# Performance work log

Hardware: AMD Instinct MI355X
Metric: run time of the kernel (lower is better)

## Reference

```python
import jax, jax.numpy as jnp
import numpy as np
import math

EMBED_DIM = 2048
NUM_HEADS = 16
D_K = 128
BSZ = 2
SEQ = 2048


def make_freq_pos_enc(dim, max_seq_len):
    # inv_freq over dim/2 freqs, then interleave-repeat each freq twice: (f r), r=2
    inv_freq = 1.0 / (10000.0 ** (jnp.arange(0, dim, 2, dtype=jnp.float32) / dim))
    pos = jnp.arange(max_seq_len, dtype=jnp.float32)
    pe = jnp.einsum('p,f->pf', pos, inv_freq)                 # [S, dim/2]
    return jnp.repeat(pe, 2, axis=-1)                          # [S, dim], pattern (f r)


def rotate_half(u):
    # pairs are interleaved: (..., d r) with r=2
    u = u.reshape(*u.shape[:-1], -1, 2)
    u1, u2 = u[..., 0], u[..., 1]
    return jnp.stack((-u2, u1), axis=-1).reshape(*u.shape[:-2], -1)


def rotate(u, pos_enc):
    pe = pos_enc[: u.shape[-2]]                                # [S, d_k]
    return u * jnp.cos(pe) + rotate_half(u) * jnp.sin(pe)


def setup_inputs() -> dict:
    key = jax.random.key(0)
    ks = jax.random.split(key, 5)
    scale = 1.0 / math.sqrt(EMBED_DIM)
    return {
        'x': jax.random.normal(ks[0], (BSZ, SEQ, EMBED_DIM), dtype=jnp.float32),
        'wq': jax.random.normal(ks[1], (NUM_HEADS * D_K, EMBED_DIM), dtype=jnp.float32) * scale,
        'wk': jax.random.normal(ks[2], (NUM_HEADS * D_K, EMBED_DIM), dtype=jnp.float32) * scale,
        'wv': jax.random.normal(ks[3], (NUM_HEADS * D_K, EMBED_DIM), dtype=jnp.float32) * scale,
        'wo': jax.random.normal(ks[4], (EMBED_DIM, NUM_HEADS * D_K), dtype=jnp.float32) * scale,
        'freq_pos_enc': make_freq_pos_enc(D_K, SEQ),
        'mask': jnp.zeros((SEQ, SEQ), dtype=jnp.float32),  # dead arg in original forward
        'num_heads': NUM_HEADS,
        'd_k': D_K,
    }


def reference(x, wq, wk, wv, wo, freq_pos_enc, mask, num_heads, d_k):
    bsz, seq_len, _ = x.shape
    # projections (nn.Linear, no bias): x @ W^T
    def proj(w):
        p = jnp.einsum('bse,de->bsd', x, w)
        return p.reshape(bsz, seq_len, num_heads, d_k).transpose(0, 2, 1, 3)  # [B,H,S,d]
    q, k, v = proj(wq), proj(wk), proj(wv)
    q, k = rotate(q, freq_pos_enc), rotate(k, freq_pos_enc)
    # regenerated causal mask (0 on/below diagonal, -inf above)
    causal = jnp.where(
        jnp.arange(seq_len)[:, None] >= jnp.arange(seq_len)[None, :],
        0.0, -jnp.inf).astype(x.dtype)
    scores = jnp.einsum('bhsd,bhtd->bhst', q, k) / math.sqrt(d_k) + causal
    weights = jax.nn.softmax(scores, axis=-1)
    attn = jnp.einsum('bhst,bhtd->bhsd', weights, v)           # [B,H,S,d]
    attn = attn.transpose(0, 2, 1, 3).reshape(bsz, seq_len, -1)
    return jnp.einsum('bsd,ed->bse', attn, wo)


if __name__ == '__main__':
    out = reference(**setup_inputs())
    print(out.shape, out.dtype)
```

## Files before the change

### kernel.cpp

```cpp
#include <hip/hip_runtime.h>


typedef unsigned short u16;
typedef unsigned int   u32;
typedef __attribute__((ext_vector_type(4)))  float f32x4;
typedef __attribute__((ext_vector_type(16))) float f32x16;
typedef __attribute__((ext_vector_type(8)))  short short8;
typedef __attribute__((ext_vector_type(4)))  u16   u16x4;
typedef __attribute__((ext_vector_type(2)))  u16   u16x2;

#define NB   2
#define NH   16
#define SEQ  2048
#define DK   128
#define EMB  2048

__device__ __forceinline__ u16 f2bf(float f) {
    union { float f; unsigned int u; } v; v.f = f;
    unsigned int r = v.u + 0x7FFFu + ((v.u >> 16) & 1u);
    return (u16)(r >> 16);
}
__device__ __forceinline__ float bf2f(u16 h) {
    union { unsigned int u; float f; } v; v.u = ((unsigned int)h) << 16;
    return v.f;
}
__device__ __forceinline__ f32x4 mfma16(short8 a, short8 b, f32x4 c) {
    return __builtin_amdgcn_mfma_f32_16x16x32_bf16(a, b, c, 0, 0, 0);
}
__device__ __forceinline__ f32x16 mfma32(short8 a, short8 b, f32x16 c) {
    return __builtin_amdgcn_mfma_f32_32x32x16_bf16(a, b, c, 0, 0, 0);
}

#define GLDS(gsrc, ldst) __builtin_amdgcn_global_load_lds( \
    (const __attribute__((address_space(1))) void*)(gsrc), \
    (__attribute__((address_space(3))) void*)(ldst), 16, 0, 0)

__global__ __launch_bounds__(256) void cast_f32_bf16(const float* __restrict__ in,
                                                     u16* __restrict__ out, int n4) {
    int i = blockIdx.x * 256 + threadIdx.x;
    if (i >= n4) return;
    f32x4 v = ((const f32x4*)in)[i];
    u16x4 o;
    o[0] = f2bf(v[0]); o[1] = f2bf(v[1]); o[2] = f2bf(v[2]); o[3] = f2bf(v[3]);
    ((u16x4*)out)[i] = o;
}

__global__ __launch_bounds__(256) void rope_table(const float* __restrict__ freq,
                                                  float* __restrict__ ct,
                                                  float* __restrict__ st) {
    int i = blockIdx.x * 256 + threadIdx.x;
    int s = i >> 6, d2 = i & 63;
    float pe = freq[s * DK + d2 * 2];
    ct[i] = cosf(pe);
    st[i] = sinf(pe);
}

__global__ __launch_bounds__(256) void rope_apply(u16* __restrict__ Qb, u16* __restrict__ Kb,
                                                  const float* __restrict__ ct,
                                                  const float* __restrict__ st) {
    int i = blockIdx.x * 256 + threadIdx.x;
    int d2 = i & 63;
    int s  = (i >> 6) & (SEQ - 1);
    float c  = ct[(s << 6) + d2];
    float sn = st[(s << 6) + d2];
    size_t off = (size_t)i * 2;
    u16x2 q = *(const u16x2*)(Qb + off);
    float q0 = bf2f(q[0]), q1 = bf2f(q[1]);
    u16x2 qo; qo[0] = f2bf(q0 * c - q1 * sn); qo[1] = f2bf(q1 * c + q0 * sn);
    *(u16x2*)(Qb + off) = qo;
    u16x2 k = *(const u16x2*)(Kb + off);
    float k0 = bf2f(k[0]), k1 = bf2f(k[1]);
    u16x2 ko; ko[0] = f2bf(k0 * c - k1 * sn); ko[1] = f2bf(k1 * c + k0 * sn);
    *(u16x2*)(Kb + off) = ko;
}

template <int MODE>
__global__ __launch_bounds__(256) void gemm_ring(const u16* __restrict__ A,
                                                 const u16* __restrict__ B,
                                                 void* __restrict__ Cout,
                                                 int M, int N, int K) {
    __shared__ __align__(16) u16 As[3 * 4096];
    __shared__ __align__(16) u16 Bs[3 * 4096];
    const int tid  = threadIdx.x;
    const int lane = tid & 63;
    const int wid  = tid >> 6;
    const int wm   = wid >> 1, wn = wid & 1;
    const int nwgx = (int)gridDim.x;
    const int wgid = (int)blockIdx.y * nwgx + (int)blockIdx.x;
    const int cpx  = (nwgx * (int)gridDim.y) >> 3;
    const int swz  = (wgid & 7) * cpx + (wgid >> 3);
    const int m0   = (swz % nwgx) * 128, n0 = (swz / nwgx) * 128;
    const int lr   = lane & 15, lk = lane >> 4;

    const u16* Asrc = A + (size_t)(m0 + (tid >> 2)) * K + (tid & 3) * 8;
    const u16* Bsrc = B + (size_t)(n0 + (tid >> 2)) * K + (tid & 3) * 8;
    const int  dst0 = wid * 512;

    f32x4 acc[4][4] = {};
    const int NT = K >> 5;

#pragma unroll
    for (int i = 0; i < 2; ++i) {
        GLDS(Asrc + (size_t)i * 64 * K,      &As[i * 2048 + dst0]);
        GLDS(Bsrc + (size_t)i * 64 * K,      &Bs[i * 2048 + dst0]);
    }
#pragma unroll
    for (int i = 0; i < 2; ++i) {
        GLDS(Asrc + (size_t)i * 64 * K + 32, &As[4096 + i * 2048 + dst0]);
        GLDS(Bsrc + (size_t)i * 64 * K + 32, &Bs[4096 + i * 2048 + dst0]);
    }

    int buf = 0;
    for (int t = 0; t < NT; ++t) {
        if (t < NT - 1) asm volatile("s_waitcnt vmcnt(4)" ::: "memory");
        else            asm volatile("s_waitcnt vmcnt(0)" ::: "memory");
        __builtin_amdgcn_s_barrier();

        short8 af[4], bf[4];
#pragma unroll
        for (int i = 0; i < 4; ++i)
            af[i] = *(const short8*)&As[buf * 4096 + (wm * 64 + i * 16 + lr) * 32 + lk * 8];
#pragma unroll
        for (int j = 0; j < 4; ++j)
            bf[j] = *(const short8*)&Bs[buf * 4096 + (wn * 64 + j * 16 + lr) * 32 + lk * 8];

        if (t + 2 < NT) {
            int b2 = buf + 2; if (b2 >= 3) b2 -= 3;
            const u16* a2  = Asrc + (size_t)(t + 2) * 32;
            const u16* b2p = Bsrc + (size_t)(t + 2) * 32;
#pragma unroll
            for (int i = 0; i < 2; ++i) {
                GLDS(a2  + (size_t)i * 64 * K, &As[b2 * 4096 + i * 2048 + dst0]);
                GLDS(b2p + (size_t)i * 64 * K, &Bs[b2 * 4096 + i * 2048 + dst0]);
            }
        }

        __builtin_amdgcn_s_setprio(1);
#pragma unroll
        for (int i = 0; i < 4; ++i)
#pragma unroll
            for (int j = 0; j < 4; ++j)
                acc[i][j] = mfma16(af[i], bf[j], acc[i][j]);
        __builtin_amdgcn_s_setprio(0);

        buf = (buf == 2) ? 0 : buf + 1;
    }

#pragma unroll
    for (int i = 0; i < 4; ++i) {
#pragma unroll
        for (int j = 0; j < 4; ++j) {
#pragma unroll
            for (int r = 0; r < 4; ++r) {
                int m = m0 + wm * 64 + i * 16 + lk * 4 + r;
                int n = n0 + wn * 64 + j * 16 + lr;
                float v = acc[i][j][r];
                if (MODE == 0) {
                    int b = m >> 11, s = m & (SEQ - 1), h = n >> 7, d = n & (DK - 1);
                    ((u16*)Cout)[(((size_t)(b * NH + h) * SEQ + s) * DK) + d] = f2bf(v);
                } else if (MODE == 1) {
                    int h = m >> 7, d = m & (DK - 1), b = n >> 11, s = n & (SEQ - 1);
                    ((u16*)Cout)[(((size_t)(b * NH + h) * DK + d) * SEQ) + s] = f2bf(v);
                } else {
                    ((float*)Cout)[(size_t)m * N + n] = v;
                }
            }
        }
    }
}

__global__ __launch_bounds__(128, 2) void attn_lds2(const u16* __restrict__ Q,
                                                    const u16* __restrict__ K,
                                                    const u16* __restrict__ VT,
                                                    u16* __restrict__ O) {
    const int gid  = blockIdx.x;
    const int bh   = (gid & 7) * 4 + ((gid >> 3) & 3);
    const int p    = gid >> 5;
    const int tid  = threadIdx.x;
    const int w    = tid >> 6;
    const int l    = tid & 63;
    const int q32  = l & 31;
    const int half = l >> 5;
    const int qcL  = 63 - p;
    const int qc   = w ? p : qcL;
    const int nt   = qcL + 1;
    const int q0   = qc * 32;

    __shared__ __align__(16) u16 Ksh[2][4096];
    __shared__ __align__(16) u16 Vsh[2][4096];

    const u16* Kg  = K  + (size_t)bh * SEQ * DK;
    const u16* VTg = VT + (size_t)bh * DK * SEQ;
    const int b = bh >> 4, h = bh & 15;

    auto stage = [&](int t, int bufn) {
#pragma unroll
        for (int i = 0; i < 4; ++i) {
            int cid = i * 128 + w * 64 + l;
            int kr = cid >> 4, kc = cid & 15;
            GLDS(Kg + (size_t)(t * 32 + kr) * DK + ((kc ^ (kr & 7)) * 8),
                 &Ksh[bufn][(i * 128 + w * 64) * 8]);
            int vr = cid >> 2, vc = cid & 3;
            GLDS(VTg + (size_t)vr * SEQ + t * 32 + ((vc ^ ((vr >> 1) & 3)) * 8),
                 &Vsh[bufn][(i * 128 + w * 64) * 8]);
        }
    };

    short8 qf[8];
    {
        const u16* Qg = Q + ((size_t)bh * SEQ + q0) * DK;
#pragma unroll
        for (int kq = 0; kq < 8; ++kq)
            qf[kq] = *(const short8*)(Qg + q32 * DK + kq * 16 + half * 8);
    }

    f32x16 oacc[4] = {};
    float m = -INFINITY, lsum = 0.f;

    stage(0, 0);
    stage(1, 1);
    for (int t = 0; t < nt; ++t) {
        const int buf = t & 1;
        if (t + 1 < nt) asm volatile("s_waitcnt vmcnt(8)" ::: "memory");
        else            asm volatile("s_waitcnt vmcnt(0)" ::: "memory");
        __builtin_amdgcn_s_barrier();
        __builtin_amdgcn_sched_barrier(0);

        if (t <= qc) {
            const float rs = 0.08838834764831845f;
            short8 kf[8], vf[8];
#pragma unroll
            for (int kq = 0; kq < 8; ++kq) {
                int c = (kq * 2 + half) ^ (q32 & 7);
                kf[kq] = *(const short8*)&Ksh[buf][q32 * 128 + c * 8];
            }
#pragma unroll
            for (int i = 0; i < 8; ++i) {
                int dblk = i >> 1, ch = i & 1;
                int vrow = dblk * 32 + q32;
                int c = (ch * 2 + half) ^ ((q32 >> 1) & 3);
                vf[i] = *(const short8*)&Vsh[buf][vrow * 32 + c * 8];
            }
            const bool diag = (t == qc);

            f32x16 sacc = {};
            __builtin_amdgcn_s_setprio(1);
#pragma unroll
            for (int kq = 0; kq < 8; ++kq) sacc = mfma32(kf[kq], qf[kq], sacc);
            __builtin_amdgcn_s_setprio(0);
#pragma unroll
            for (int r = 0; r < 16; ++r) {
                int kk = (r & 3) + 8 * (r >> 2) + 4 * half;
                float s = sacc[r] * rs;
                if (diag && kk > q32) s = -INFINITY;
                sacc[r] = s;
            }
            float mx[8];
#pragma unroll
            for (int r = 0; r < 8; ++r) mx[r] = fmaxf(sacc[r], sacc[r + 8]);
#pragma unroll
            for (int r = 0; r < 4; ++r) mx[r] = fmaxf(mx[r], mx[r + 4]);
            float tmax = fmaxf(fmaxf(mx[0], mx[1]), fmaxf(mx[2], mx[3]));
            tmax = fmaxf(tmax, __shfl_xor(tmax, 32));
            if (__any(tmax - m > 8.0f)) {
                float mn = fmaxf(m, tmax);
                float sc = __expf(m - mn);
                m = mn; lsum *= sc;
#pragma unroll
                for (int d = 0; d < 4; ++d)
#pragma unroll
                    for (int r = 0; r < 16; ++r) oacc[d][r] *= sc;
            }
#pragma unroll
            for (int r = 0; r < 16; ++r) sacc[r] = __expf(sacc[r] - m);
            float sm[8];
#pragma unroll
            for (int r = 0; r < 8; ++r) sm[r] = sacc[r] + sacc[r + 8];
#pragma unroll
            for (int r = 0; r < 4; ++r) sm[r] = sm[r] + sm[r + 4];
            float tsum = (sm[0] + sm[1]) + (sm[2] + sm[3]);
            tsum += __shfl_xor(tsum, 32);
            lsum += tsum;
            u32 pk[8];
#pragma unroll
            for (int i = 0; i < 8; ++i)
                pk[i] = ((u32)f2bf(sacc[2 * i + 1]) << 16) | (u32)f2bf(sacc[2 * i]);
            u32 s0 = __shfl_xor((int)pk[0], 32), s1 = __shfl_xor((int)pk[1], 32);
            u32 s2 = __shfl_xor((int)pk[2], 32), s3 = __shfl_xor((int)pk[3], 32);
            u32 s4 = __shfl_xor((int)pk[4], 32), s5 = __shfl_xor((int)pk[5], 32);
            u32 s6 = __shfl_xor((int)pk[6], 32), s7 = __shfl_xor((int)pk[7], 32);
            union { u32 wd[4]; short8 s8; } P0, P1;
            P0.wd[0] = half ? s2    : pk[0];  P0.wd[1] = half ? s3    : pk[1];
            P0.wd[2] = half ? pk[2] : s0;     P0.wd[3] = half ? pk[3] : s1;
            P1.wd[0] = half ? s6    : pk[4];  P1.wd[1] = half ? s7    : pk[5];
            P1.wd[2] = half ? pk[6] : s4;     P1.wd[3] = half ? pk[7] : s5;
            __builtin_amdgcn_s_setprio(1);
#pragma unroll
            for (int d = 0; d < 4; ++d) {
                oacc[d] = mfma32(vf[2 * d],     P0.s8, oacc[d]);
                oacc[d] = mfma32(vf[2 * d + 1], P1.s8, oacc[d]);
            }
            __builtin_amdgcn_s_setprio(0);
        }

        __builtin_amdgcn_s_barrier();
        if (t + 2 < nt) stage(t + 2, buf);
    }

    float inv = 1.0f / lsum;
    u16* Og = O + ((size_t)b * SEQ + q0 + q32) * EMB + h * DK;
#pragma unroll
    for (int d = 0; d < 4; ++d)
#pragma unroll
        for (int rq = 0; rq < 4; ++rq) {
            u16x4 o4;
#pragma unroll
            for (int j = 0; j < 4; ++j) o4[j] = f2bf(oacc[d][rq * 4 + j] * inv);
            *(u16x4*)(Og + d * 32 + rq * 8 + half * 4) = o4;
        }
}

extern "C" void kernel_launch(void* const* d_in, const int* in_sizes, int n_in,
                              void* d_out, int out_size, void* d_ws, size_t ws_size,
                              hipStream_t stream) {
    const float* x    = (const float*)d_in[0];
    const float* wq   = (const float*)d_in[1];
    const float* wk   = (const float*)d_in[2];
    const float* wv   = (const float*)d_in[3];
    const float* wo   = (const float*)d_in[4];
    const float* freq = (const float*)d_in[5];

    char* ws = (char*)d_ws;
    u16*  xb  = (u16*)(ws);
    u16*  wqb = (u16*)(ws + 16777216);
    u16*  wkb = (u16*)(ws + 25165824);
    u16*  wvb = (u16*)(ws + 33554432);
    u16*  wob = (u16*)(ws + 41943040);
    u16*  Qb  = (u16*)(ws + 50331648);
    u16*  Kb  = (u16*)(ws + 67108864);
    u16*  VTb = (u16*)(ws + 83886080);
    float* ct = (float*)(ws + 100663296);
    float* st = (float*)(ws + 101187584);
    u16*  attn = xb;

    cast_f32_bf16<<<8192, 256, 0, stream>>>(x,  xb,  2097152);
    cast_f32_bf16<<<4096, 256, 0, stream>>>(wq, wqb, 1048576);
    cast_f32_bf16<<<4096, 256, 0, stream>>>(wk, wkb, 1048576);
    cast_f32_bf16<<<4096, 256, 0, stream>>>(wv, wvb, 1048576);
    cast_f32_bf16<<<4096, 256, 0, stream>>>(wo, wob, 1048576);
    rope_table<<<512, 256, 0, stream>>>(freq, ct, st);

    gemm_ring<0><<<dim3(32, 16), 256, 0, stream>>>(xb,  wqb, Qb,  4096, 2048, 2048);
    gemm_ring<0><<<dim3(32, 16), 256, 0, stream>>>(xb,  wkb, Kb,  4096, 2048, 2048);
    gemm_ring<1><<<dim3(16, 32), 256, 0, stream>>>(wvb, xb,  VTb, 2048, 4096, 2048);

    rope_apply<<<16384, 256, 0, stream>>>(Qb, Kb, ct, st);

    attn_lds2<<<1024, 128, 0, stream>>>(Qb, Kb, VTb, attn);

    gemm_ring<3><<<dim3(32, 16), 256, 0, stream>>>(attn, wob, d_out, 4096, 2048, 2048);
}
```

Before: 294.5 us.

## Use 64-key tiles with adjacent query-chunk pairs in attention; merge weight casts

The attention kernel now pairs two adjacent 32-row query chunks per block and stages 64-key K/V tiles, replacing the earlier pairing of a long and a short chunk. This halves the number of loop iterations and barriers per block and lets both waves share each staged tile, at the cost of doubled LDS per buffer and more registers. Blocks are launched in reverse order so the longest ones start first. Separately, the four weight-cast launches are merged into a single kernel to cut launch overhead.

```diff
diff --git a/kernel.cpp b/kernel.cpp
--- a/kernel.cpp
+++ b/kernel.cpp
@@ -43,6 +43,23 @@
     u16x4 o;
     o[0] = f2bf(v[0]); o[1] = f2bf(v[1]); o[2] = f2bf(v[2]); o[3] = f2bf(v[3]);
     ((u16x4*)out)[i] = o;
+}
+
+__global__ __launch_bounds__(256) void cast_weights(const float* __restrict__ wq,
+                                                    const float* __restrict__ wk,
+                                                    const float* __restrict__ wv,
+                                                    const float* __restrict__ wo,
+                                                    u16* __restrict__ oq, u16* __restrict__ ok,
+                                                    u16* __restrict__ ov, u16* __restrict__ oo) {
+    int i   = blockIdx.x * 256 + threadIdx.x;
+    int sel = i >> 20;
+    int idx = i & 1048575;
+    const float* src = (sel == 0) ? wq : (sel == 1) ? wk : (sel == 2) ? wv : wo;
+    u16*         dst = (sel == 0) ? oq : (sel == 1) ? ok : (sel == 2) ? ov : oo;
+    f32x4 v = ((const f32x4*)src)[idx];
+    u16x4 o;
+    o[0] = f2bf(v[0]); o[1] = f2bf(v[1]); o[2] = f2bf(v[2]); o[3] = f2bf(v[3]);
+    ((u16x4*)dst)[idx] = o;
 }
 
 __global__ __launch_bounds__(256) void rope_table(const float* __restrict__ freq,
@@ -169,46 +186,45 @@
     }
 }
 
-__global__ __launch_bounds__(128, 2) void attn_lds2(const u16* __restrict__ Q,
-                                                    const u16* __restrict__ K,
-                                                    const u16* __restrict__ VT,
-                                                    u16* __restrict__ O) {
+__global__ __launch_bounds__(128, 2) void attn64(const u16* __restrict__ Q,
+                                                 const u16* __restrict__ K,
+                                                 const u16* __restrict__ VT,
+                                                 u16* __restrict__ O) {
     const int gid  = blockIdx.x;
     const int bh   = (gid & 7) * 4 + ((gid >> 3) & 3);
-    const int p    = gid >> 5;
+    const int p    = 31 - (gid >> 5);
     const int tid  = threadIdx.x;
     const int w    = tid >> 6;
     const int l    = tid & 63;
     const int q32  = l & 31;
     const int half = l >> 5;
-    const int qcL  = 63 - p;
-    const int qc   = w ? p : qcL;
-    const int nt   = qcL + 1;
-    const int q0   = qc * 32;
-
-    __shared__ __align__(16) u16 Ksh[2][4096];
-    __shared__ __align__(16) u16 Vsh[2][4096];
+    const int qc   = 2 * p + w;
+    const int q    = qc * 32 + q32;
+    const int nt   = p + 1;
+
+    __shared__ __align__(16) u16 Ksh[2][8192];
+    __shared__ __align__(16) u16 Vsh[2][8192];
 
     const u16* Kg  = K  + (size_t)bh * SEQ * DK;
     const u16* VTg = VT + (size_t)bh * DK * SEQ;
     const int b = bh >> 4, h = bh & 15;
 
-    auto stage = [&](int t, int bufn) {
-#pragma unroll
-        for (int i = 0; i < 4; ++i) {
+    auto stage = [&](int T, int bufn) {
+#pragma unroll
+        for (int i = 0; i < 8; ++i) {
             int cid = i * 128 + w * 64 + l;
             int kr = cid >> 4, kc = cid & 15;
-            GLDS(Kg + (size_t)(t * 32 + kr) * DK + ((kc ^ (kr & 7)) * 8),
+            GLDS(Kg + (size_t)(T * 64 + kr) * DK + ((kc ^ (kr & 7)) * 8),
                  &Ksh[bufn][(i * 128 + w * 64) * 8]);
-            int vr = cid >> 2, vc = cid & 3;
-            GLDS(VTg + (size_t)vr * SEQ + t * 32 + ((vc ^ ((vr >> 1) & 3)) * 8),
+            int vr = cid >> 3, vc = cid & 7;
+            GLDS(VTg + (size_t)vr * SEQ + T * 64 + ((vc ^ (vr & 7)) * 8),
                  &Vsh[bufn][(i * 128 + w * 64) * 8]);
         }
     };
 
     short8 qf[8];
     {
-        const u16* Qg = Q + ((size_t)bh * SEQ + q0) * DK;
+        const u16* Qg = Q + ((size_t)bh * SEQ + qc * 32) * DK;
 #pragma unroll
         for (int kq = 0; kq < 8; ++kq)
             qf[kq] = *(const short8*)(Qg + q32 * DK + kq * 16 + half * 8);
@@ -221,94 +237,140 @@
     stage(1, 1);
     for (int t = 0; t < nt; ++t) {
         const int buf = t & 1;
-        if (t + 1 < nt) asm volatile("s_waitcnt vmcnt(8)" ::: "memory");
+        if (t + 1 < nt) asm volatile("s_waitcnt vmcnt(16)" ::: "memory");
         else            asm volatile("s_waitcnt vmcnt(0)" ::: "memory");
         __builtin_amdgcn_s_barrier();
         __builtin_amdgcn_sched_barrier(0);
 
-        if (t <= qc) {
-            const float rs = 0.08838834764831845f;
-            short8 kf[8], vf[8];
+        const float rs = 0.08838834764831845f;
+        const bool diag = (t == p);
+        const bool doH1 = !(diag && w == 0);
+
+        short8 kf[8];
+#pragma unroll
+        for (int kq = 0; kq < 8; ++kq) {
+            int c = (kq * 2 + half) ^ (q32 & 7);
+            kf[kq] = *(const short8*)&Ksh[buf][q32 * 128 + c * 8];
+        }
+        f32x16 sacc0 = {};
+        __builtin_amdgcn_s_setprio(1);
+#pragma unroll
+        for (int kq = 0; kq < 8; ++kq) sacc0 = mfma32(kf[kq], qf[kq], sacc0);
+        __builtin_amdgcn_s_setprio(0);
+
+        f32x16 sacc1 = {};
+        if (doH1) {
 #pragma unroll
             for (int kq = 0; kq < 8; ++kq) {
                 int c = (kq * 2 + half) ^ (q32 & 7);
-                kf[kq] = *(const short8*)&Ksh[buf][q32 * 128 + c * 8];
+                kf[kq] = *(const short8*)&Ksh[buf][(32 + q32) * 128 + c * 8];
             }
-#pragma unroll
-            for (int i = 0; i < 8; ++i) {
-                int dblk = i >> 1, ch = i & 1;
-                int vrow = dblk * 32 + q32;
-                int c = (ch * 2 + half) ^ ((q32 >> 1) & 3);
-                vf[i] = *(const short8*)&Vsh[buf][vrow * 32 + c * 8];
+            __builtin_amdgcn_s_setprio(1);
+#pragma unroll
+            for (int kq = 0; kq < 8; ++kq) sacc1 = mfma32(kf[kq], qf[kq], sacc1);
+            __builtin_amdgcn_s_setprio(0);
+        }
+
+#pragma unroll
+        for (int r = 0; r < 16; ++r) {
+            int kk = 64 * t + (r & 3) + 8 * (r >> 2) + 4 * half;
+            float s0 = sacc0[r] * rs;
+            if (diag && kk > q) s0 = -INFINITY;
+            sacc0[r] = s0;
+            float s1 = sacc1[r] * rs;
+            if (diag && kk + 32 > q) s1 = -INFINITY;
+            sacc1[r] = s1;
+        }
+
+        float mx[8];
+#pragma unroll
+        for (int r = 0; r < 8; ++r) mx[r] = fmaxf(sacc0[r], sacc0[r + 8]);
+        if (doH1) {
+#pragma unroll
+            for (int r = 0; r < 8; ++r) mx[r] = fmaxf(mx[r], fmaxf(sacc1[r], sacc1[r + 8]));
+        }
+#pragma unroll
+        for (int r = 0; r < 4; ++r) mx[r] = fmaxf(mx[r], mx[r + 4]);
+        float tmax = fmaxf(fmaxf(mx[0], mx[1]), fmaxf(mx[2], mx[3]));
+        tmax = fmaxf(tmax, __shfl_xor(tmax, 32));
+        if (__any(tmax - m > 8.0f)) {
+            float mn = fmaxf(m, tmax);
+            float sc = __expf(m - mn);
+            m = mn; lsum *= sc;
+#pragma unroll
+            for (int d = 0; d < 4; ++d)
+#pragma unroll
+                for (int r = 0; r < 16; ++r) oacc[d][r] *= sc;
+        }
+#pragma unroll
+        for (int r = 0; r < 16; ++r) sacc0[r] = __expf(sacc0[r] - m);
+        if (doH1) {
+#pragma unroll
+            for (int r = 0; r < 16; ++r) sacc1[r] = __expf(sacc1[r] - m);
+        }
+        float sm[8];
+#pragma unroll
+        for (int r = 0; r < 8; ++r) sm[r] = sacc0[r] + sacc0[r + 8];
+        if (doH1) {
+#pragma unroll
+            for (int r = 0; r < 8; ++r) sm[r] += sacc1[r] + sacc1[r + 8];
+        }
+#pragma unroll
+        for (int r = 0; r < 4; ++r) sm[r] = sm[r] + sm[r + 4];
+        float tsum = (sm[0] + sm[1]) + (sm[2] + sm[3]);
+        tsum += __shfl_xor(tsum, 32);
+        lsum += tsum;
+
+        u32 pk[8];
+#pragma unroll
+        for (int i = 0; i < 8; ++i)
+            pk[i] = ((u32)f2bf(sacc0[2 * i + 1]) << 16) | (u32)f2bf(sacc0[2 * i]);
+        u32 s0 = __shfl_xor((int)pk[0], 32), s1 = __shfl_xor((int)pk[1], 32);
+        u32 s2 = __shfl_xor((int)pk[2], 32), s3 = __shfl_xor((int)pk[3], 32);
+        u32 s4 = __shfl_xor((int)pk[4], 32), s5 = __shfl_xor((int)pk[5], 32);
+        u32 s6 = __shfl_xor((int)pk[6], 32), s7 = __shfl_xor((int)pk[7], 32);
+        union { u32 wd[4]; short8 s8; } P0, P1, P2, P3;
+        P0.wd[0] = half ? s2    : pk[0];  P0.wd[1] = half ? s3    : pk[1];
+        P0.wd[2] = half ? pk[2] : s0;     P0.wd[3] = half ? pk[3] : s1;
+        P1.wd[0] = half ? s6    : pk[4];  P1.wd[1] = half ? s7    : pk[5];
+        P1.wd[2] = half ? pk[6] : s4;     P1.wd[3] = half ? pk[7] : s5;
+        if (doH1) {
+#pragma unroll
+            for (int i = 0; i < 8; ++i)
+                pk[i] = ((u32)f2bf(sacc1[2 * i + 1]) << 16) | (u32)f2bf(sacc1[2 * i]);
+            u32 t0 = __shfl_xor((int)pk[0], 32), t1 = __shfl_xor((int)pk[1], 32);
+            u32 t2 = __shfl_xor((int)pk[2], 32), t3 = __shfl_xor((int)pk[3], 32);
+            u32 t4 = __shfl_xor((int)pk[4], 32), t5 = __shfl_xor((int)pk[5], 32);
+            u32 t6 = __shfl_xor((int)pk[6], 32), t7 = __shfl_xor((int)pk[7], 32);
+            P2.wd[0] = half ? t2    : pk[0];  P2.wd[1] = half ? t3    : pk[1];
+            P2.wd[2] = half ? pk[2] : t0;     P2.wd[3] = half ? pk[3] : t1;
+            P3.wd[0] = half ? t6    : pk[4];  P3.wd[1] = half ? t7    : pk[5];
+            P3.wd[2] = half ? pk[6] : t4;     P3.wd[3] = half ? pk[7] : t5;
+        }
+
+        __builtin_amdgcn_s_setprio(1);
+#pragma unroll
+        for (int d = 0; d < 4; ++d) {
+            int vrow = d * 32 + q32;
+            short8 v0 = *(const short8*)&Vsh[buf][vrow * 64 + (((0 * 2 + half) ^ (q32 & 7)) * 8)];
+            short8 v1 = *(const short8*)&Vsh[buf][vrow * 64 + (((1 * 2 + half) ^ (q32 & 7)) * 8)];
+            oacc[d] = mfma32(v0, P0.s8, oacc[d]);
+            oacc[d] = mfma32(v1, P1.s8, oacc[d]);
+            if (doH1) {
+                short8 v2 = *(const short8*)&Vsh[buf][vrow * 64 + (((2 * 2 + half) ^ (q32 & 7)) * 8)];
+                short8 v3 = *(const short8*)&Vsh[buf][vrow * 64 + (((3 * 2 + half) ^ (q32 & 7)) * 8)];
+                oacc[d] = mfma32(v2, P2.s8, oacc[d]);
+                oacc[d] = mfma32(v3, P3.s8, oacc[d]);
             }
-            const bool diag = (t == qc);
-
-            f32x16 sacc = {};
-            __builtin_amdgcn_s_setprio(1);
-#pragma unroll
-            for (int kq = 0; kq < 8; ++kq) sacc = mfma32(kf[kq], qf[kq], sacc);
-            __builtin_amdgcn_s_setprio(0);
-#pragma unroll
-            for (int r = 0; r < 16; ++r) {
-                int kk = (r & 3) + 8 * (r >> 2) + 4 * half;
-                float s = sacc[r] * rs;
-                if (diag && kk > q32) s = -INFINITY;
-                sacc[r] = s;
-            }
-            float mx[8];
-#pragma unroll
-            for (int r = 0; r < 8; ++r) mx[r] = fmaxf(sacc[r], sacc[r + 8]);
-#pragma unroll
-            for (int r = 0; r < 4; ++r) mx[r] = fmaxf(mx[r], mx[r + 4]);
-            float tmax = fmaxf(fmaxf(mx[0], mx[1]), fmaxf(mx[2], mx[3]));
-            tmax = fmaxf(tmax, __shfl_xor(tmax, 32));
-            if (__any(tmax - m > 8.0f)) {
-                float mn = fmaxf(m, tmax);
-                float sc = __expf(m - mn);
-                m = mn; lsum *= sc;
-#pragma unroll
-                for (int d = 0; d < 4; ++d)
-#pragma unroll
-                    for (int r = 0; r < 16; ++r) oacc[d][r] *= sc;
-            }
-#pragma unroll
-            for (int r = 0; r < 16; ++r) sacc[r] = __expf(sacc[r] - m);
-            float sm[8];
-#pragma unroll
-            for (int r = 0; r < 8; ++r) sm[r] = sacc[r] + sacc[r + 8];
-#pragma unroll
-            for (int r = 0; r < 4; ++r) sm[r] = sm[r] + sm[r + 4];
-            float tsum = (sm[0] + sm[1]) + (sm[2] + sm[3]);
-            tsum += __shfl_xor(tsum, 32);
-            lsum += tsum;
-            u32 pk[8];
-#pragma unroll
-            for (int i = 0; i < 8; ++i)
-                pk[i] = ((u32)f2bf(sacc[2 * i + 1]) << 16) | (u32)f2bf(sacc[2 * i]);
-            u32 s0 = __shfl_xor((int)pk[0], 32), s1 = __shfl_xor((int)pk[1], 32);
-            u32 s2 = __shfl_xor((int)pk[2], 32), s3 = __shfl_xor((int)pk[3], 32);
-            u32 s4 = __shfl_xor((int)pk[4], 32), s5 = __shfl_xor((int)pk[5], 32);
-            u32 s6 = __shfl_xor((int)pk[6], 32), s7 = __shfl_xor((int)pk[7], 32);
-            union { u32 wd[4]; short8 s8; } P0, P1;
-            P0.wd[0] = half ? s2    : pk[0];  P0.wd[1] = half ? s3    : pk[1];
-            P0.wd[2] = half ? pk[2] : s0;     P0.wd[3] = half ? pk[3] : s1;
-            P1.wd[0] = half ? s6    : pk[4];  P1.wd[1] = half ? s7    : pk[5];
-            P1.wd[2] = half ? pk[6] : s4;     P1.wd[3] = half ? pk[7] : s5;
-            __builtin_amdgcn_s_setprio(1);
-#pragma unroll
-            for (int d = 0; d < 4; ++d) {
-                oacc[d] = mfma32(vf[2 * d],     P0.s8, oacc[d]);
-                oacc[d] = mfma32(vf[2 * d + 1], P1.s8, oacc[d]);
-            }
-            __builtin_amdgcn_s_setprio(0);
-        }
+        }
+        __builtin_amdgcn_s_setprio(0);
 
         __builtin_amdgcn_s_barrier();
         if (t + 2 < nt) stage(t + 2, buf);
     }
 
     float inv = 1.0f / lsum;
-    u16* Og = O + ((size_t)b * SEQ + q0 + q32) * EMB + h * DK;
+    u16* Og = O + ((size_t)b * SEQ + qc * 32 + q32) * EMB + h * DK;
 #pragma unroll
     for (int d = 0; d < 4; ++d)
 #pragma unroll
@@ -343,11 +405,8 @@
     float* st = (float*)(ws + 101187584);
     u16*  attn = xb;
 
-    cast_f32_bf16<<<8192, 256, 0, stream>>>(x,  xb,  2097152);
-    cast_f32_bf16<<<4096, 256, 0, stream>>>(wq, wqb, 1048576);
-    cast_f32_bf16<<<4096, 256, 0, stream>>>(wk, wkb, 1048576);
-    cast_f32_bf16<<<4096, 256, 0, stream>>>(wv, wvb, 1048576);
-    cast_f32_bf16<<<4096, 256, 0, stream>>>(wo, wob, 1048576);
+    cast_f32_bf16<<<8192, 256, 0, stream>>>(x, xb, 2097152);
+    cast_weights<<<16384, 256, 0, stream>>>(wq, wk, wv, wo, wqb, wkb, wvb, wob);
     rope_table<<<512, 256, 0, stream>>>(freq, ct, st);
 
     gemm_ring<0><<<dim3(32, 16), 256, 0, stream>>>(xb,  wqb, Qb,  4096, 2048, 2048);
@@ -356,7 +415,7 @@
 
     rope_apply<<<16384, 256, 0, stream>>>(Qb, Kb, ct, st);
 
-    attn_lds2<<<1024, 128, 0, stream>>>(Qb, Kb, VTb, attn);
+    attn64<<<1024, 128, 0, stream>>>(Qb, Kb, VTb, attn);
 
     gemm_ring<3><<<dim3(32, 16), 256, 0, stream>>>(attn, wob, d_out, 4096, 2048, 2048);
 }
```

New measurement: 294.3 us. No clear change (-0.1%).

## Fuse RoPE into Q/K GEMM epilogue, merge weight casts, reorder attention chunks

Applied to the files above, without the earlier changes.

Applies the rotary embedding inside the Q/K projection GEMM epilogue, using a lane shuffle to fetch the paired element, and drops the separate rope_apply pass over Q and K. The four weight-cast launches are merged into one kernel. The attention kernel now gives each block two adjacent query chunks and launches the heavy blocks first, instead of pairing a long and a short chunk. This trades the earlier per-block causal balance for scheduling-based balance and adds table loads to the GEMM epilogue.

```diff
diff --git a/kernel.cpp b/kernel.cpp
--- a/kernel.cpp
+++ b/kernel.cpp
@@ -45,6 +45,23 @@
     ((u16x4*)out)[i] = o;
 }
 
+__global__ __launch_bounds__(256) void cast_weights(const float* __restrict__ wq,
+                                                    const float* __restrict__ wk,
+                                                    const float* __restrict__ wv,
+                                                    const float* __restrict__ wo,
+                                                    u16* __restrict__ oq, u16* __restrict__ ok,
+                                                    u16* __restrict__ ov, u16* __restrict__ oo) {
+    int i   = blockIdx.x * 256 + threadIdx.x;
+    int sel = i >> 20;
+    int idx = i & 1048575;
+    const float* src = (sel == 0) ? wq : (sel == 1) ? wk : (sel == 2) ? wv : wo;
+    u16*         dst = (sel == 0) ? oq : (sel == 1) ? ok : (sel == 2) ? ov : oo;
+    f32x4 v = ((const f32x4*)src)[idx];
+    u16x4 o;
+    o[0] = f2bf(v[0]); o[1] = f2bf(v[1]); o[2] = f2bf(v[2]); o[3] = f2bf(v[3]);
+    ((u16x4*)dst)[idx] = o;
+}
+
 __global__ __launch_bounds__(256) void rope_table(const float* __restrict__ freq,
                                                   float* __restrict__ ct,
                                                   float* __restrict__ st) {
@@ -55,30 +72,13 @@
     st[i] = sinf(pe);
 }
 
-__global__ __launch_bounds__(256) void rope_apply(u16* __restrict__ Qb, u16* __restrict__ Kb,
-                                                  const float* __restrict__ ct,
-                                                  const float* __restrict__ st) {
-    int i = blockIdx.x * 256 + threadIdx.x;
-    int d2 = i & 63;
-    int s  = (i >> 6) & (SEQ - 1);
-    float c  = ct[(s << 6) + d2];
-    float sn = st[(s << 6) + d2];
-    size_t off = (size_t)i * 2;
-    u16x2 q = *(const u16x2*)(Qb + off);
-    float q0 = bf2f(q[0]), q1 = bf2f(q[1]);
-    u16x2 qo; qo[0] = f2bf(q0 * c - q1 * sn); qo[1] = f2bf(q1 * c + q0 * sn);
-    *(u16x2*)(Qb + off) = qo;
-    u16x2 k = *(const u16x2*)(Kb + off);
-    float k0 = bf2f(k[0]), k1 = bf2f(k[1]);
-    u16x2 ko; ko[0] = f2bf(k0 * c - k1 * sn); ko[1] = f2bf(k1 * c + k0 * sn);
-    *(u16x2*)(Kb + off) = ko;
-}
-
 template <int MODE>
 __global__ __launch_bounds__(256) void gemm_ring(const u16* __restrict__ A,
                                                  const u16* __restrict__ B,
                                                  void* __restrict__ Cout,
-                                                 int M, int N, int K) {
+                                                 int M, int N, int K,
+                                                 const float* __restrict__ ct,
+                                                 const float* __restrict__ st) {
     __shared__ __align__(16) u16 As[3 * 4096];
     __shared__ __align__(16) u16 Bs[3 * 4096];
     const int tid  = threadIdx.x;
@@ -161,6 +161,13 @@
                 } else if (MODE == 1) {
                     int h = m >> 7, d = m & (DK - 1), b = n >> 11, s = n & (SEQ - 1);
                     ((u16*)Cout)[(((size_t)(b * NH + h) * DK + d) * SEQ) + s] = f2bf(v);
+                } else if (MODE == 6) {
+                    int b = m >> 11, s = m & (SEQ - 1), h = n >> 7, d = n & (DK - 1);
+                    float part = __shfl_xor(v, 1);
+                    int ti = (s << 6) + (d >> 1);
+                    float c = ct[ti], sn = st[ti];
+                    float vr = (lr & 1) ? (v * c + part * sn) : (v * c - part * sn);
+                    ((u16*)Cout)[(((size_t)(b * NH + h) * SEQ + s) * DK) + d] = f2bf(vr);
                 } else {
                     ((float*)Cout)[(size_t)m * N + n] = v;
                 }
@@ -175,15 +182,14 @@
                                                     u16* __restrict__ O) {
     const int gid  = blockIdx.x;
     const int bh   = (gid & 7) * 4 + ((gid >> 3) & 3);
-    const int p    = gid >> 5;
+    const int p    = 31 - (gid >> 5);
     const int tid  = threadIdx.x;
     const int w    = tid >> 6;
     const int l    = tid & 63;
     const int q32  = l & 31;
     const int half = l >> 5;
-    const int qcL  = 63 - p;
-    const int qc   = w ? p : qcL;
-    const int nt   = qcL + 1;
+    const int qc   = 2 * p + w;
+    const int nt   = 2 * p + 2;
     const int q0   = qc * 32;
 
     __shared__ __align__(16) u16 Ksh[2][4096];
@@ -343,20 +349,15 @@
     float* st = (float*)(ws + 101187584);
     u16*  attn = xb;
 
-    cast_f32_bf16<<<8192, 256, 0, stream>>>(x,  xb,  2097152);
-    cast_f32_bf16<<<4096, 256, 0, stream>>>(wq, wqb, 1048576);
-    cast_f32_bf16<<<4096, 256, 0, stream>>>(wk, wkb, 1048576);
-    cast_f32_bf16<<<4096, 256, 0, stream>>>(wv, wvb, 1048576);
-    cast_f32_bf16<<<4096, 256, 0, stream>>>(wo, wob, 1048576);
+    cast_f32_bf16<<<8192, 256, 0, stream>>>(x, xb, 2097152);
+    cast_weights<<<16384, 256, 0, stream>>>(wq, wk, wv, wo, wqb, wkb, wvb, wob);
     rope_table<<<512, 256, 0, stream>>>(freq, ct, st);
 
-    gemm_ring<0><<<dim3(32, 16), 256, 0, stream>>>(xb,  wqb, Qb,  4096, 2048, 2048);
-    gemm_ring<0><<<dim3(32, 16), 256, 0, stream>>>(xb,  wkb, Kb,  4096, 2048, 2048);
-    gemm_ring<1><<<dim3(16, 32), 256, 0, stream>>>(wvb, xb,  VTb, 2048, 4096, 2048);
-
-    rope_apply<<<16384, 256, 0, stream>>>(Qb, Kb, ct, st);
+    gemm_ring<6><<<dim3(32, 16), 256, 0, stream>>>(xb,  wqb, Qb,  4096, 2048, 2048, ct, st);
+    gemm_ring<6><<<dim3(32, 16), 256, 0, stream>>>(xb,  wkb, Kb,  4096, 2048, 2048, ct, st);
+    gemm_ring<1><<<dim3(16, 32), 256, 0, stream>>>(wvb, xb,  VTb, 2048, 4096, 2048, nullptr, nullptr);
 
     attn_lds2<<<1024, 128, 0, stream>>>(Qb, Kb, VTb, attn);
 
-    gemm_ring<3><<<dim3(32, 16), 256, 0, stream>>>(attn, wob, d_out, 4096, 2048, 2048);
-}
+    gemm_ring<3><<<dim3(32, 16), 256, 0, stream>>>(attn, wob, d_out, 4096, 2048, 2048, nullptr, nullptr);
+}
```

After: 285.4 us. 1.03x faster.
